# Performance work log

Hardware: AMD Instinct MI355X
Metric: run time of the kernel (lower is better)

The kernel has to match this reference:

```python
import jax, jax.numpy as jnp
import numpy as np

B, T, FEAT, FUSION, H, C = 128, 64, 4096, 1024, 1024, 2


def setup_inputs() -> dict:
    key = jax.random.key(0)
    ks = jax.random.split(key, 9)
    s_feat = 1.0 / np.sqrt(FEAT)
    s_h = 1.0 / np.sqrt(H)
    return {
        "x": jax.random.normal(ks[0], (B, T, FEAT), jnp.float32),
        "W_feat": jax.random.normal(ks[1], (FUSION, FEAT), jnp.float32) * s_feat,
        "b_feat": jax.random.normal(ks[2], (FUSION,), jnp.float32) * s_feat,
        "W_ih": jax.random.normal(ks[3], (4 * H, FUSION), jnp.float32) * s_h,
        "b_ih": jax.random.normal(ks[4], (4 * H,), jnp.float32) * s_h,
        "W_hh": jax.random.normal(ks[5], (4 * H, H), jnp.float32) * s_h,
        "b_hh": jax.random.normal(ks[6], (4 * H,), jnp.float32) * s_h,
        "W_cls": jax.random.normal(ks[7], (C, H), jnp.float32) * s_h,
        "b_cls": jax.random.normal(ks[8], (C,), jnp.float32) * s_h,
    }


def reference(x, W_feat, b_feat, W_ih, b_ih, W_hh, b_hh, W_cls, b_cls):
    # x: [B, T, FEAT]. Sequential LSTMCell loop expressed as lax.scan over time.
    Hdim = W_hh.shape[1]
    Bb = x.shape[0]
    h0 = jnp.zeros((Bb, Hdim), x.dtype)
    c0 = jnp.zeros((Bb, Hdim), x.dtype)

    def step(carry, x_t):
        h, c = carry
        # feature extractor: Linear + ReLU fusion (dropout = identity in eval)
        f = jax.nn.relu(x_t @ W_feat.T + b_feat)  # [B, FUSION]
        gates = f @ W_ih.T + b_ih + h @ W_hh.T + b_hh  # [B, 4H]
        i, fg, g, o = jnp.split(gates, 4, axis=-1)  # torch LSTMCell gate order
        i = jax.nn.sigmoid(i)
        fg = jax.nn.sigmoid(fg)
        g = jnp.tanh(g)
        o = jax.nn.sigmoid(o)
        c_new = fg * c + i * g
        h_new = o * jnp.tanh(c_new)
        s = h_new @ W_cls.T + b_cls  # [B, 2]
        return (h_new, c_new), s

    xs = jnp.swapaxes(x, 0, 1)  # [T, B, FEAT]
    _, scores = jax.lax.scan(step, (h0, c0), xs)  # [T, B, 2]
    return jnp.swapaxes(scores, 0, 1)  # [B, T, 2]
```

## Files before the change

### kernel.cpp

```cpp
#include <hip/hip_runtime.h>
#include <math.h>


typedef __attribute__((ext_vector_type(8))) short short8v;
typedef __attribute__((ext_vector_type(4))) float f32x4;
typedef unsigned short u16;

#define HF2_BUF 262144
#define HF2_MT  32768
#define GX_PLANE 8388608u

__device__ __forceinline__ short f2h(float f) {
    return __builtin_bit_cast(short, (_Float16)f);
}
__device__ __forceinline__ float h2f(u16 h) {
    return (float)__builtin_bit_cast(_Float16, (short)h);
}

__global__ void cvt_f16(const float* __restrict__ src, u16* __restrict__ d, int n4) {
    int i = blockIdx.x * blockDim.x + threadIdx.x;
    if (i >= n4) return;
    float4 v = ((const float4*)src)[i];
    ushort4 o;
    o.x = (u16)f2h(v.x); o.y = (u16)f2h(v.y);
    o.z = (u16)f2h(v.z); o.w = (u16)f2h(v.w);
    ((ushort4*)d)[i] = o;
}

__global__ void prep_misc(float* __restrict__ out, const float* __restrict__ b_cls,
                          const float* __restrict__ b_ih, const float* __restrict__ b_hh,
                          float* __restrict__ bsum) {
    int i = blockIdx.x * blockDim.x + threadIdx.x;
    if (i < 16384) out[i] = b_cls[i & 1];
    if (i < 4096)  bsum[i] = b_ih[i] + b_hh[i];
}

__global__ __launch_bounds__(512)
void gemm_a512(const float* __restrict__ Af, int lda,
               const u16* __restrict__ B16, int ldb,
               const float* __restrict__ bias,
               u16* __restrict__ C16, int ldc, int K)
{
    __shared__ short8v As[16][64];
    __shared__ short8v Bs[16][64];

    const int tid = threadIdx.x;
    const int l   = tid & 63;
    const int w   = tid >> 6;
    const int wm  = w & 1, wn = w >> 1;
    const int bm  = blockIdx.x * 128, bn = blockIdx.y * 128;

    const int sm    = tid >> 2;
    const int sk8   = (tid & 3) * 8;
    const int koct_s = sk8 >> 3;
    const int slane = ((sm & 15) ^ (koct_s << 1)) | (koct_s << 4);
    const int smf   = sm >> 4;
    const int lsw   = ((l & 15) ^ ((l >> 4) << 1)) | (l & 48);

    f32x4 acc[4][2];
#pragma unroll
    for (int i = 0; i < 4; ++i)
#pragma unroll
        for (int j = 0; j < 2; ++j)
#pragma unroll
            for (int r = 0; r < 4; ++r) acc[i][j][r] = 0.f;

    for (int k0 = 0; k0 < K; k0 += 64) {
#pragma unroll
        for (int h = 0; h < 2; ++h) {
            const int kk = k0 + h * 32 + sk8;
            float fa[8];
            const float* p0 = Af + (size_t)(bm + sm) * lda + kk;
            *(float4*)(fa)     = *(const float4*)(p0);
            *(float4*)(fa + 4) = *(const float4*)(p0 + 4);
            short8v ha;
#pragma unroll
            for (int e = 0; e < 8; ++e) ha[e] = f2h(fa[e]);
            As[h * 8 + smf][slane] = ha;
            Bs[h * 8 + smf][slane] = *(const short8v*)(B16 + (size_t)(bn + sm) * ldb + kk);
        }
        __syncthreads();

#pragma unroll
        for (int h = 0; h < 2; ++h) {
            short8v a[4];
#pragma unroll
            for (int i = 0; i < 4; ++i) a[i] = As[h * 8 + wm * 4 + i][lsw];
#pragma unroll
            for (int j = 0; j < 2; ++j) {
                const short8v b = Bs[h * 8 + wn * 2 + j][lsw];
#pragma unroll
                for (int i = 0; i < 4; ++i)
                    acc[i][j] = __builtin_amdgcn_mfma_f32_16x16x32_f16(a[i], b, acc[i][j], 0, 0, 0);
            }
        }
        __syncthreads();
    }

    const int row0 = bm + wm * 64 + (l >> 4) * 4;
    const int col0 = bn + wn * 32 + (l & 15);
#pragma unroll
    for (int i = 0; i < 4; ++i) {
#pragma unroll
        for (int j = 0; j < 2; ++j) {
            const int col = col0 + j * 16;
            const float bs = bias[col];
#pragma unroll
            for (int r = 0; r < 4; ++r) {
                const int row = row0 + i * 16 + r;
                float v = fmaxf(acc[i][j][r] + bs, 0.f);
                C16[(size_t)row * ldc + col] = (u16)f2h(v);
            }
        }
    }
}

__global__ __launch_bounds__(256)
void gemm_b(const u16* __restrict__ A16, int lda,
            const u16* __restrict__ B16, int ldb,
            const float* __restrict__ bias,
            u16* __restrict__ C16, int K)
{
    __shared__ short8v As[16][64];
    __shared__ short8v Bs[16][64];

    const int tid = threadIdx.x;
    const int l   = tid & 63;
    const int w   = tid >> 6;
    const int wm  = w & 1, wn = w >> 1;
    const int bm  = blockIdx.x * 128, bn = blockIdx.y * 128;

    const int sm    = tid >> 2;
    const int sk8   = (tid & 3) * 8;
    const int koct_s = sk8 >> 3;
    const int slane = ((sm & 15) ^ (koct_s << 1)) | (koct_s << 4);
    const int smf   = sm >> 4;
    const int lsw   = ((l & 15) ^ ((l >> 4) << 1)) | (l & 48);

    f32x4 acc[4][4];
#pragma unroll
    for (int i = 0; i < 4; ++i)
#pragma unroll
        for (int j = 0; j < 4; ++j)
#pragma unroll
            for (int r = 0; r < 4; ++r) acc[i][j][r] = 0.f;

    for (int k0 = 0; k0 < K; k0 += 64) {
#pragma unroll
        for (int h = 0; h < 2; ++h) {
            const int kk = k0 + h * 32 + sk8;
            As[h * 8 + smf][slane]     = *(const short8v*)(A16 + (size_t)(bm + sm) * lda + kk);
            As[h * 8 + smf + 4][slane] = *(const short8v*)(A16 + (size_t)(bm + sm + 64) * lda + kk);
            Bs[h * 8 + smf][slane]     = *(const short8v*)(B16 + (size_t)(bn + sm) * ldb + kk);
            Bs[h * 8 + smf + 4][slane] = *(const short8v*)(B16 + (size_t)(bn + sm + 64) * ldb + kk);
        }
        __syncthreads();

#pragma unroll
        for (int h = 0; h < 2; ++h) {
            short8v a[4];
#pragma unroll
            for (int i = 0; i < 4; ++i) a[i] = As[h * 8 + wm * 4 + i][lsw];
#pragma unroll
            for (int j = 0; j < 4; ++j) {
                const short8v b = Bs[h * 8 + wn * 4 + j][lsw];
#pragma unroll
                for (int i = 0; i < 4; ++i)
                    acc[i][j] = __builtin_amdgcn_mfma_f32_16x16x32_f16(a[i], b, acc[i][j], 0, 0, 0);
            }
        }
        __syncthreads();
    }

    const int row0 = bm + wm * 64 + (l >> 4) * 4;
    const int col0 = bn + wn * 64 + (l & 15);
#pragma unroll
    for (int i = 0; i < 4; ++i) {
#pragma unroll
        for (int j = 0; j < 4; ++j) {
            const int col = col0 + j * 16;
            const float bs = bias[col];
#pragma unroll
            for (int r = 0; r < 4; ++r) {
                const int row = row0 + i * 16 + r;
                const float v = acc[i][j][r] + bs;
                const size_t rr = (size_t)(row & 63) * 128 + (row >> 6);
                C16[(size_t)(col >> 10) * GX_PLANE + rr * 1024 + (col & 1023)]
                    = (u16)f2h(v);
            }
        }
    }
}

__global__ void pack_whh3(const float* __restrict__ W, char* __restrict__ Wf) {
    int gid = blockIdx.x * blockDim.x + threadIdx.x;
    int l = gid & 63, fid = gid >> 6;
    int kcl = fid & 15, kh = (fid >> 4) & 1, ngrp = (fid >> 5) & 63, g = fid >> 11;
    int n = g * 1024 + ngrp * 16 + (l & 15);
    int k = kh * 512 + kcl * 32 + (l >> 4) * 8;
    const float* src = W + (size_t)n * 1024 + k;
    short8v v16;
#pragma unroll
    for (int e = 0; e < 8; ++e) v16[e] = f2h(src[e]);
    *(short8v*)(Wf + (size_t)fid * 1024 + (size_t)l * 16) = v16;
}

__global__ __launch_bounds__(512)
void lstm_step(const u16* __restrict__ Gxp,
               const char*  __restrict__ Wf,
               char*        __restrict__ hfrag,
               float*       __restrict__ c,
               const float* __restrict__ Wc,
               float*       __restrict__ out,
               int t)
{
    __shared__ short8v Hs[64][64];
    __shared__ float gates_s[2][4][32][16];
    __shared__ float h_s[32][16];
    __shared__ float Wc_s[2][16];

    const int tid = threadIdx.x, bid = blockIdx.x;
    const int w = tid >> 6, l = tid & 63;
    const int g = w & 3, kh = w >> 2;
    const int ngrp = bid & 63, mh = bid >> 6;

    const int r_c  = tid >> 4;
    const int cw_c = tid & 15;
    const int row_c = mh * 32 + r_c;
    const int col_c = ngrp * 16 + cw_c;
    const u16* gp = Gxp + ((size_t)t * 128 + row_c) * 1024 + col_c;
    const u16 gv0 = gp[0];
    const u16 gv1 = gp[GX_PLANE];
    const u16 gv2 = gp[2u * GX_PLANE];
    const u16 gv3 = gp[3u * GX_PLANE];
    const size_t cidx = (size_t)row_c * 1024 + col_c;
    const float cp = (t > 0) ? c[cidx] : 0.f;

    if (tid < 32) Wc_s[tid >> 4][tid & 15] =
        Wc[(size_t)(tid >> 4) * 1024 + ngrp * 16 + (tid & 15)];

    const int lhi = l >> 4;
    const int llo = l & 15;

    f32x4 aE0, aO0, aE1, aO1;
#pragma unroll
    for (int r = 0; r < 4; ++r) { aE0[r] = 0.f; aO0[r] = 0.f; aE1[r] = 0.f; aO1[r] = 0.f; }

    if (t > 0) {
        const char* hbase = hfrag + ((t - 1) & 1) * HF2_BUF;
#pragma unroll
        for (int it = 0; it < 8; ++it) {
            const int u  = tid + it * 512;
            const int s  = u >> 6;
            const int ln = u & 63;
            Hs[s][ln] = *(const short8v*)(hbase
                        + (size_t)(2 * mh + (s >> 5)) * HF2_MT
                        + (size_t)(s & 31) * 1024 + (size_t)ln * 16);
        }
        __syncthreads();

        const char* wb = Wf + (size_t)((g * 64 + ngrp) * 2 + kh) * 16384 + (size_t)l * 16;
#pragma unroll
        for (int kcl = 0; kcl < 16; kcl += 2) {
            const short8v b0 = *(const short8v*)(wb + kcl * 1024);
            const short8v b1 = *(const short8v*)(wb + (kcl + 1) * 1024);
            const int kc0 = kh * 16 + kcl;
            aE0 = __builtin_amdgcn_mfma_f32_16x16x32_f16(Hs[kc0][l],      b0, aE0, 0, 0, 0);
            aE1 = __builtin_amdgcn_mfma_f32_16x16x32_f16(Hs[32 + kc0][l], b0, aE1, 0, 0, 0);
            aO0 = __builtin_amdgcn_mfma_f32_16x16x32_f16(Hs[kc0 + 1][l],      b1, aO0, 0, 0, 0);
            aO1 = __builtin_amdgcn_mfma_f32_16x16x32_f16(Hs[32 + kc0 + 1][l], b1, aO1, 0, 0, 0);
        }
    }

#pragma unroll
    for (int r = 0; r < 4; ++r) {
        gates_s[kh][g][lhi * 4 + r][llo]      = aE0[r] + aO0[r];
        gates_s[kh][g][16 + lhi * 4 + r][llo] = aE1[r] + aO1[r];
    }
    __syncthreads();

    {
        float gate[4];
        gate[0] = h2f(gv0); gate[1] = h2f(gv1);
        gate[2] = h2f(gv2); gate[3] = h2f(gv3);
#pragma unroll
        for (int gg = 0; gg < 4; ++gg)
            gate[gg] += gates_s[0][gg][r_c][cw_c] + gates_s[1][gg][r_c][cw_c];
        float ig = 1.f / (1.f + __expf(-gate[0]));
        float fg = 1.f / (1.f + __expf(-gate[1]));
        float gg = tanhf(gate[2]);
        float og = 1.f / (1.f + __expf(-gate[3]));
        float cn = fg * cp + ig * gg;
        float hn = og * tanhf(cn);
        c[cidx] = cn;
        h_s[r_c][cw_c] = hn;

        float s0 = hn * Wc_s[0][cw_c];
        float s1 = hn * Wc_s[1][cw_c];
#pragma unroll
        for (int off = 8; off > 0; off >>= 1) {
            s0 += __shfl_xor(s0, off);
            s1 += __shfl_xor(s1, off);
        }
        if (cw_c == 0) {
            float* o = out + ((size_t)row_c * 64 + t) * 2;
            atomicAdd(o,     s0);
            atomicAdd(o + 1, s1);
        }
    }
    __syncthreads();

    if (tid < 64) {
        const int idx16  = tid & 15;
        const int koct_h = (tid >> 4) & 1;
        const int mt_l   = (tid >> 5) & 1;
        const int lane   = idx16 | (((ngrp & 1) * 2 + koct_h) << 4);
        short8v v;
#pragma unroll
        for (int e = 0; e < 8; ++e)
            v[e] = f2h(h_s[mt_l * 16 + idx16][koct_h * 8 + e]);
        char* dst = hfrag + (t & 1) * HF2_BUF
                  + (size_t)(2 * mh + mt_l) * HF2_MT
                  + (size_t)(ngrp >> 1) * 1024 + (size_t)lane * 16;
        *(short8v*)dst = v;
    }
}

extern "C" void kernel_launch(void* const* d_in, const int* in_sizes, int n_in,
                              void* d_out, int out_size, void* d_ws, size_t ws_size,
                              hipStream_t stream) {
    const float* x      = (const float*)d_in[0];
    const float* W_feat = (const float*)d_in[1];
    const float* b_feat = (const float*)d_in[2];
    const float* W_ih   = (const float*)d_in[3];
    const float* b_ih   = (const float*)d_in[4];
    const float* W_hh   = (const float*)d_in[5];
    const float* b_hh   = (const float*)d_in[6];
    const float* W_cls  = (const float*)d_in[7];
    const float* b_cls  = (const float*)d_in[8];
    float* out = (float*)d_out;

    char* ws = (char*)d_ws;
    u16*  F16   = (u16*)ws;
    u16*  Wih16 = (u16*)(ws + 16777216);
    u16*  Wf16  = (u16*)(ws + 25165824);
    u16*  Gxp   = (u16*)(ws + 33554432);
    float* bsum = (float*)(ws + 104857600);
    char* Wf    = ws;
    char* hfrag = ws + 16777216;
    float* c    = (float*)(ws + 17825792);

    cvt_f16<<<dim3(4096), dim3(256), 0, stream>>>(W_feat, Wf16, 1048576);
    cvt_f16<<<dim3(4096), dim3(256), 0, stream>>>(W_ih, Wih16, 1048576);
    prep_misc<<<dim3(64), dim3(256), 0, stream>>>(out, b_cls, b_ih, b_hh, bsum);

    gemm_a512<<<dim3(64, 8), 512, 0, stream>>>(
        x, 4096, Wf16, 4096, b_feat, F16, 1024, 4096);

    gemm_b<<<dim3(64, 32), 256, 0, stream>>>(
        F16, 1024, Wih16, 1024, bsum, Gxp, 1024);

    pack_whh3<<<dim3(2048), dim3(256), 0, stream>>>(W_hh, Wf);

    for (int t = 0; t < 64; ++t) {
        lstm_step<<<dim3(256), dim3(512), 0, stream>>>(
            Gxp, Wf, hfrag, c, W_cls, out, t);
    }
}
```

Before: 656.2 us.

## Split LSTM step into 512 blocks of 16 rows, merge weight conversions

The per-timestep LSTM kernel changes from 256 blocks of 512 threads, each covering 32 batch rows with a K-split across two wave groups, to 512 blocks of 256 threads, each covering 16 rows and the full K range. This drops the K-split reduction through shared memory and puts more blocks on the device to fill the CUs during the latency-bound recurrent steps. The cost is that each W_hh fragment is now read by twice as many blocks. Separately, the two fp32-to-fp16 weight conversion launches are merged into one.

```diff
diff --git a/kernel.cpp b/kernel.cpp
--- a/kernel.cpp
+++ b/kernel.cpp
@@ -17,14 +17,17 @@
     return (float)__builtin_bit_cast(_Float16, (short)h);
 }
 
-__global__ void cvt_f16(const float* __restrict__ src, u16* __restrict__ d, int n4) {
+__global__ void cvt_both(const float* __restrict__ wfeat, u16* __restrict__ dfeat,
+                         const float* __restrict__ wih, u16* __restrict__ dih) {
     int i = blockIdx.x * blockDim.x + threadIdx.x;
-    if (i >= n4) return;
-    float4 v = ((const float4*)src)[i];
+    const float* src = (i < 1048576) ? wfeat : wih;
+    u16* dst = (i < 1048576) ? dfeat : dih;
+    int j = i & 1048575;
+    float4 v = ((const float4*)src)[j];
     ushort4 o;
     o.x = (u16)f2h(v.x); o.y = (u16)f2h(v.y);
     o.z = (u16)f2h(v.z); o.w = (u16)f2h(v.w);
-    ((ushort4*)d)[i] = o;
+    ((ushort4*)dst)[j] = o;
 }
 
 __global__ void prep_misc(float* __restrict__ out, const float* __restrict__ b_cls,
@@ -205,7 +208,7 @@
     *(short8v*)(Wf + (size_t)fid * 1024 + (size_t)l * 16) = v16;
 }
 
-__global__ __launch_bounds__(512)
+__global__ __launch_bounds__(256)
 void lstm_step(const u16* __restrict__ Gxp,
                const char*  __restrict__ Wf,
                char*        __restrict__ hfrag,
@@ -214,19 +217,18 @@
                float*       __restrict__ out,
                int t)
 {
-    __shared__ short8v Hs[64][64];
-    __shared__ float gates_s[2][4][32][16];
-    __shared__ float h_s[32][16];
+    __shared__ short8v Hs[32][64];
+    __shared__ float gates_s[4][16][16];
+    __shared__ float h_s[16][16];
     __shared__ float Wc_s[2][16];
 
     const int tid = threadIdx.x, bid = blockIdx.x;
-    const int w = tid >> 6, l = tid & 63;
-    const int g = w & 3, kh = w >> 2;
-    const int ngrp = bid & 63, mh = bid >> 6;
+    const int g = tid >> 6, l = tid & 63;
+    const int ngrp = bid & 63, mt = bid >> 6;
 
     const int r_c  = tid >> 4;
     const int cw_c = tid & 15;
-    const int row_c = mh * 32 + r_c;
+    const int row_c = mt * 16 + r_c;
     const int col_c = ngrp * 16 + cw_c;
     const u16* gp = Gxp + ((size_t)t * 128 + row_c) * 1024 + col_c;
     const u16 gv0 = gp[0];
@@ -242,41 +244,34 @@
     const int lhi = l >> 4;
     const int llo = l & 15;
 
-    f32x4 aE0, aO0, aE1, aO1;
-#pragma unroll
-    for (int r = 0; r < 4; ++r) { aE0[r] = 0.f; aO0[r] = 0.f; aE1[r] = 0.f; aO1[r] = 0.f; }
+    f32x4 aE, aO;
+#pragma unroll
+    for (int r = 0; r < 4; ++r) { aE[r] = 0.f; aO[r] = 0.f; }
 
     if (t > 0) {
-        const char* hbase = hfrag + ((t - 1) & 1) * HF2_BUF;
+        const char* hbase = hfrag + ((t - 1) & 1) * HF2_BUF + (size_t)mt * HF2_MT;
 #pragma unroll
         for (int it = 0; it < 8; ++it) {
-            const int u  = tid + it * 512;
+            const int u  = tid + it * 256;
             const int s  = u >> 6;
             const int ln = u & 63;
-            Hs[s][ln] = *(const short8v*)(hbase
-                        + (size_t)(2 * mh + (s >> 5)) * HF2_MT
-                        + (size_t)(s & 31) * 1024 + (size_t)ln * 16);
-        }
-        __syncthreads();
-
-        const char* wb = Wf + (size_t)((g * 64 + ngrp) * 2 + kh) * 16384 + (size_t)l * 16;
-#pragma unroll
-        for (int kcl = 0; kcl < 16; kcl += 2) {
+            Hs[s][ln] = *(const short8v*)(hbase + (size_t)s * 1024 + (size_t)ln * 16);
+        }
+        __syncthreads();
+
+        const char* wb = Wf + ((size_t)(g * 64 + ngrp) * 32) * 1024 + (size_t)l * 16;
+#pragma unroll
+        for (int kcl = 0; kcl < 32; kcl += 2) {
             const short8v b0 = *(const short8v*)(wb + kcl * 1024);
             const short8v b1 = *(const short8v*)(wb + (kcl + 1) * 1024);
-            const int kc0 = kh * 16 + kcl;
-            aE0 = __builtin_amdgcn_mfma_f32_16x16x32_f16(Hs[kc0][l],      b0, aE0, 0, 0, 0);
-            aE1 = __builtin_amdgcn_mfma_f32_16x16x32_f16(Hs[32 + kc0][l], b0, aE1, 0, 0, 0);
-            aO0 = __builtin_amdgcn_mfma_f32_16x16x32_f16(Hs[kc0 + 1][l],      b1, aO0, 0, 0, 0);
-            aO1 = __builtin_amdgcn_mfma_f32_16x16x32_f16(Hs[32 + kc0 + 1][l], b1, aO1, 0, 0, 0);
-        }
-    }
-
-#pragma unroll
-    for (int r = 0; r < 4; ++r) {
-        gates_s[kh][g][lhi * 4 + r][llo]      = aE0[r] + aO0[r];
-        gates_s[kh][g][16 + lhi * 4 + r][llo] = aE1[r] + aO1[r];
-    }
+            aE = __builtin_amdgcn_mfma_f32_16x16x32_f16(Hs[kcl][l],     b0, aE, 0, 0, 0);
+            aO = __builtin_amdgcn_mfma_f32_16x16x32_f16(Hs[kcl + 1][l], b1, aO, 0, 0, 0);
+        }
+    }
+
+#pragma unroll
+    for (int r = 0; r < 4; ++r)
+        gates_s[g][lhi * 4 + r][llo] = aE[r] + aO[r];
     __syncthreads();
 
     {
@@ -285,7 +280,7 @@
         gate[2] = h2f(gv2); gate[3] = h2f(gv3);
 #pragma unroll
         for (int gg = 0; gg < 4; ++gg)
-            gate[gg] += gates_s[0][gg][r_c][cw_c] + gates_s[1][gg][r_c][cw_c];
+            gate[gg] += gates_s[gg][r_c][cw_c];
         float ig = 1.f / (1.f + __expf(-gate[0]));
         float fg = 1.f / (1.f + __expf(-gate[1]));
         float gg = tanhf(gate[2]);
@@ -310,17 +305,15 @@
     }
     __syncthreads();
 
-    if (tid < 64) {
+    if (tid < 32) {
         const int idx16  = tid & 15;
-        const int koct_h = (tid >> 4) & 1;
-        const int mt_l   = (tid >> 5) & 1;
+        const int koct_h = tid >> 4;
         const int lane   = idx16 | (((ngrp & 1) * 2 + koct_h) << 4);
         short8v v;
 #pragma unroll
         for (int e = 0; e < 8; ++e)
-            v[e] = f2h(h_s[mt_l * 16 + idx16][koct_h * 8 + e]);
-        char* dst = hfrag + (t & 1) * HF2_BUF
-                  + (size_t)(2 * mh + mt_l) * HF2_MT
+            v[e] = f2h(h_s[idx16][koct_h * 8 + e]);
+        char* dst = hfrag + (t & 1) * HF2_BUF + (size_t)mt * HF2_MT
                   + (size_t)(ngrp >> 1) * 1024 + (size_t)lane * 16;
         *(short8v*)dst = v;
     }
@@ -350,8 +343,7 @@
     char* hfrag = ws + 16777216;
     float* c    = (float*)(ws + 17825792);
 
-    cvt_f16<<<dim3(4096), dim3(256), 0, stream>>>(W_feat, Wf16, 1048576);
-    cvt_f16<<<dim3(4096), dim3(256), 0, stream>>>(W_ih, Wih16, 1048576);
+    cvt_both<<<dim3(8192), dim3(256), 0, stream>>>(W_feat, Wf16, W_ih, Wih16);
     prep_misc<<<dim3(64), dim3(256), 0, stream>>>(out, b_cls, b_ih, b_hh, bsum);
 
     gemm_a512<<<dim3(64, 8), 512, 0, stream>>>(
@@ -363,7 +355,7 @@
     pack_whh3<<<dim3(2048), dim3(256), 0, stream>>>(W_hh, Wf);
 
     for (int t = 0; t < 64; ++t) {
-        lstm_step<<<dim3(256), dim3(512), 0, stream>>>(
+        lstm_step<<<dim3(512), dim3(256), 0, stream>>>(
             Gxp, Wf, hfrag, c, W_cls, out, t);
     }
 }
```

Measured after the change: 703.6 us. +7.2%, slower.
